# Kernel optimization log

Measured on AMD Instinct MI355X. Metric: run time of the kernel, lower is better.

## Reference

```python
import jax, jax.numpy as jnp
import numpy as np

CONF_THRES = 0.96
IOU_THRES = 0.45
MAX_CAND = 2048        # fixed candidate cap (jit-static stand-in for data-dependent nonzero)
DET_PER_IMG = 300
AGNOSTIC = False
LABEL_OFF = 4.0        # class offset for batched NMS; boxes lie within [-0.5, 1.5]


def _cxcywh_to_xyxy(b):
    cx, cy, w, h = b[..., 0], b[..., 1], b[..., 2], b[..., 3]
    return jnp.stack([cx - 0.5 * w, cy - 0.5 * h, cx + 0.5 * w, cy + 0.5 * h], axis=-1)


def _box_iou(a, b):
    # a: [K,4], b: [K,4] -> [K,K]
    lt = jnp.maximum(a[:, None, :2], b[None, :, :2])
    rb = jnp.minimum(a[:, None, 2:], b[None, :, 2:])
    wh = jnp.clip(rb - lt, 0.0)
    inter = wh[..., 0] * wh[..., 1]
    area_a = (a[:, 2] - a[:, 0]) * (a[:, 3] - a[:, 1])
    area_b = (b[:, 2] - b[:, 0]) * (b[:, 3] - b[:, 1])
    return inter / (area_a[:, None] + area_b[None, :] - inter + 1e-9)


def _process_image(x, nc):
    # x: [N, 5+nc]
    obj = x[:, 4]
    cls_scores = x[:, 5:] * obj[:, None]                 # x[:,5:] *= x[:,4:5]
    boxes = _cxcywh_to_xyxy(x[:, :4])                    # [N,4]
    # multi-label candidates: (obj > conf) pre-filter, then (obj*cls > conf)
    cand_mask = (cls_scores > CONF_THRES) & (obj[:, None] > CONF_THRES)
    flat_scores = jnp.where(cand_mask, cls_scores, -1.0).reshape(-1)  # [N*nc]
    top_scores, top_idx = jax.lax.top_k(flat_scores, MAX_CAND)        # sorted desc
    anchor = top_idx // nc
    label = top_idx % nc
    cand_boxes = boxes[anchor]                           # [K,4]
    valid = top_scores > 0.0

    # batched (class-aware) NMS via per-class coordinate offset
    if AGNOSTIC:
        nms_boxes = cand_boxes
    else:
        nms_boxes = cand_boxes + (label.astype(cand_boxes.dtype) * LABEL_OFF)[:, None]
    iou = _box_iou(nms_boxes, nms_boxes)                 # [K,K]
    idxs = jnp.arange(MAX_CAND)

    def body(i, keep):
        suppress = keep[i] & (iou[i] > IOU_THRES) & (idxs > i)
        return keep & ~suppress

    keep = jax.lax.fori_loop(0, MAX_CAND, body, valid)
    kept_scores = jnp.where(keep, top_scores, -1.0)
    det_scores, det_idx = jax.lax.top_k(kept_scores, DET_PER_IMG)
    det_valid = det_scores > 0.0
    det = jnp.concatenate(
        [cand_boxes[det_idx], det_scores[:, None], label[det_idx].astype(x.dtype)[:, None]],
        axis=1,
    )  # [DET_PER_IMG, 6] = (x1, y1, x2, y2, score, class)
    return jnp.where(det_valid[:, None], det, 0.0)


def setup_inputs() -> dict:
    key = jax.random.key(0)
    prediction = jax.random.uniform(key, (8, 25200, 85), dtype=jnp.float32)
    return {"prediction": prediction}


def reference(prediction):
    nc = prediction.shape[2] - 5
    return jax.vmap(lambda x: _process_image(x, nc))(prediction)
```

## Files before the change

kernel.cpp:

```cpp
#include <hip/hip_runtime.h>
#include <stdint.h>

#define CONF 0.96f
#define IOUT 0.45f
#define NA 25200
#define DIM 85
#define NC 80
#define NIMG 8
#define NCAND 2048
#define CAPRAW 4096
#define NDET 300
#define CH 64
#define NCH (NCAND / CH)
#define APB 112
#define NSEG (NA / APB)
#define SEGCAP 96
#define K2U 64
#define K2P 4

__global__ __launch_bounds__(128) void k1_filter(
    const float* __restrict__ pred, int* __restrict__ bcnt,
    uint64_t* __restrict__ raw_k) {
    __shared__ int   hot[APB];
    __shared__ float hobj[APB];
    __shared__ uint64_t l_k[SEGCAP];
    __shared__ int   l_hot, l_cnt;
    int tid = threadIdx.x;
    int img = blockIdx.y;
    int blk = blockIdx.x;
    int a0 = blk * APB;
    if (tid == 0) { l_hot = 0; l_cnt = 0; }
    __syncthreads();

    if (tid < APB) {
        float obj = pred[((size_t)img * NA + a0 + tid) * DIM + 4];
        if (obj > CONF) {
            int p = atomicAdd(&l_hot, 1);
            hot[p] = tid; hobj[p] = obj;
        }
    }
    __syncthreads();
    int items = l_hot * NC;
    for (int w = tid; w < items; w += 128) {
        int hi = w / NC;
        int c = w - hi * NC;
        int al = hot[hi];
        float s = pred[((size_t)img * NA + a0 + al) * DIM + 5 + c] * hobj[hi];
        if (s > CONF) {
            int q = atomicAdd(&l_cnt, 1);
            if (q < SEGCAP)
                l_k[q] = ((uint64_t)__float_as_uint(s) << 32)
                       | (uint32_t)(~(uint32_t)((a0 + al) * NC + c));
        }
    }
    __syncthreads();
    int c = l_cnt; if (c > SEGCAP) c = SEGCAP;
    if (tid == 0) bcnt[img * 256 + blk] = c;
    uint64_t* seg = raw_k + ((size_t)img * NSEG + blk) * SEGCAP;
    for (int i = tid; i < c; i += 128) seg[i] = l_k[i];
}

__global__ __launch_bounds__(256) void k2_rank(
    const float* __restrict__ pred,
    const int* __restrict__ bcnt, const uint64_t* __restrict__ raw_k,
    int* __restrict__ n_arr,
    float* __restrict__ score, int* __restrict__ label,
    float* __restrict__ ox1, float* __restrict__ oy1,
    float* __restrict__ ox2, float* __restrict__ oy2,
    float* __restrict__ area,
    float* __restrict__ rx1, float* __restrict__ ry1,
    float* __restrict__ rx2, float* __restrict__ ry2) {
    __shared__ uint64_t keys[CAPRAW];
    __shared__ int sc[256];
    __shared__ int rk[K2U][K2P];
    int img = blockIdx.y;
    int unit = blockIdx.x;
    int tid = threadIdx.x;
    int c = (tid < NSEG) ? bcnt[img * 256 + tid] : 0;
    sc[tid] = c;
    __syncthreads();
    for (int d = 1; d < 256; d <<= 1) {
        int v = (tid >= d) ? sc[tid - d] : 0;
        __syncthreads();
        sc[tid] += v;
        __syncthreads();
    }
    int total = sc[255];
    int m = total < CAPRAW ? total : CAPRAW;
    if (unit == 0 && tid == 0) n_arr[img] = m < NCAND ? m : NCAND;
    if (unit * K2U >= m) return;

    int off = sc[tid] - c;
    const uint64_t* seg = raw_k + ((size_t)img * NSEG + tid) * SEGCAP;
    for (int k = 0; k < c; ++k) {
        int pos = off + k;
        if (pos < CAPRAW) keys[pos] = seg[k];
    }
    for (int j = tid; j < CAPRAW; j += 256)
        if (j >= m) keys[j] = 0;
    __syncthreads();

    int cand = tid & (K2U - 1);
    int part = tid >> 6;
    int idx = unit * K2U + cand;
    bool valid = idx < m;
    uint64_t my = keys[idx];
    int mt = (m + 7) & ~7;
    int q = ((mt + 31) >> 5) << 3;
    int lo = part * q;
    int hi = lo + q; if (hi > mt) hi = mt;
    int r = 0;
#pragma unroll 8
    for (int j = lo; j < hi; ++j) r += (keys[j] > my) ? 1 : 0;
    rk[cand][part] = r;
    __syncthreads();
    if (part == 0) {
        int rank = rk[cand][0] + rk[cand][1] + rk[cand][2] + rk[cand][3];
        if (valid && rank < NCAND) {
            float s = __uint_as_float((uint32_t)(my >> 32));
            uint32_t myf = ~((uint32_t)my);
            int anchor = (int)(myf / NC);
            int lab = (int)(myf - (uint32_t)anchor * NC);
            const float* p = pred + ((size_t)img * NA + anchor) * DIM;
            float cx = p[0], cy = p[1], wv = p[2], hv = p[3];
            float x1 = cx - 0.5f * wv, y1 = cy - 0.5f * hv;
            float x2 = cx + 0.5f * wv, y2 = cy + 0.5f * hv;
            float offl = (float)lab * 4.0f;
            size_t o = (size_t)img * NCAND + rank;
            score[o] = s; label[o] = lab;
            rx1[o] = x1; ry1[o] = y1; rx2[o] = x2; ry2[o] = y2;
            float o1 = x1 + offl, o2 = y1 + offl, o3 = x2 + offl, o4 = y2 + offl;
            ox1[o] = o1; oy1[o] = o2; ox2[o] = o3; oy2[o] = o4;
            area[o] = (o3 - o1) * (o4 - o2);
        }
    }
}

__global__ __launch_bounds__(64) void k3_mask(
    const int* __restrict__ n_arr,
    const float* __restrict__ ox1, const float* __restrict__ oy1,
    const float* __restrict__ ox2, const float* __restrict__ oy2,
    const float* __restrict__ area, uint64_t* __restrict__ mask64) {
    __shared__ float jx1[CH], jy1[CH], jx2[CH], jy2[CH], jar[CH];
    int img = blockIdx.y;
    int n = n_arr[img];
    int ci = blockIdx.x >> 5, cj = blockIdx.x & 31;
    int t = threadIdx.x;
    size_t base = (size_t)img * NCAND;
    int i = ci * CH + t;
    uint64_t w = 0;
    if (cj >= ci && ci * CH < n && cj * CH < n) {
        {
            int j = cj * CH + t;
            float x1 = 0.f, y1 = 0.f, x2 = 0.f, y2 = 0.f, ar = 0.f;
            if (j < n) {
                x1 = ox1[base + j]; y1 = oy1[base + j];
                x2 = ox2[base + j]; y2 = oy2[base + j]; ar = area[base + j];
            }
            jx1[t] = x1; jy1[t] = y1; jx2[t] = x2; jy2[t] = y2; jar[t] = ar;
        }
        __syncthreads();
        float ax1 = 0.f, ay1 = 0.f, ax2 = 0.f, ay2 = 0.f, aar = 0.f;
        if (i < n) {
            ax1 = ox1[base + i]; ay1 = oy1[base + i];
            ax2 = ox2[base + i]; ay2 = oy2[base + i]; aar = area[base + i];
        }
        int jg0 = cj * CH;
#pragma unroll 8
        for (int jj = 0; jj < CH; ++jj) {
            float ltx = fmaxf(ax1, jx1[jj]), lty = fmaxf(ay1, jy1[jj]);
            float rbx = fminf(ax2, jx2[jj]), rby = fminf(ay2, jy2[jj]);
            float ww = fmaxf(rbx - ltx, 0.f), hh = fmaxf(rby - lty, 0.f);
            float inter = ww * hh;
            float iou = inter / (aar + jar[jj] - inter + 1e-9f);
            w |= (iou > IOUT && (jg0 + jj) > i) ? (1ull << jj) : 0ull;
        }
    }
    mask64[(base + (size_t)i) * NCH + cj] = w;
}

__global__ void k4_scan(const int* __restrict__ n_arr,
                        const uint32_t* __restrict__ mask,
                        const float* __restrict__ score, const int* __restrict__ label,
                        const float* __restrict__ rx1, const float* __restrict__ ry1,
                        const float* __restrict__ rx2, const float* __restrict__ ry2,
                        float* __restrict__ out) {
    int img = blockIdx.x;
    int lane = threadIdx.x;
    int n = n_arr[img];
    size_t cbase = (size_t)img * NCAND;
    const uint32_t* rowp = mask + cbase * 64 + lane;
    float* outp = out + (size_t)img * NDET * 6;

    uint32_t removed = 0;
    int kcnt = 0;
    constexpr int PF = 32;
    uint32_t buf[PF];
#pragma unroll
    for (int k = 0; k < PF; ++k) buf[k] = rowp[(size_t)k * 64];
    for (int ib = 0; ib < n; ib += PF) {
#pragma unroll
        for (int k = 0; k < PF; ++k) {
            int i = ib + k;
            uint32_t row = buf[k];
            int pi = i + PF; if (pi > NCAND - 1) pi = NCAND - 1;
            buf[k] = rowp[(size_t)pi * 64];
            uint32_t w = (uint32_t)__builtin_amdgcn_readlane((int)removed, i >> 5);
            uint32_t kept = ((w >> (i & 31)) & 1u) ^ 1u;
            kcnt += (int)kept;
            removed |= row & (0u - kept);
        }
        if (kcnt >= NDET) break;
    }

    int j0 = lane << 5;
    uint32_t vmask = (j0 + 32 <= n) ? 0xffffffffu
                   : (j0 >= n ? 0u : ((1u << (n - j0)) - 1u));
    uint32_t keptw = ~removed & vmask;
    int cntk = __popc(keptw);
    int pre = cntk;
    for (int d = 1; d < 64; d <<= 1) {
        int tv = __shfl_up(pre, d);
        if (lane >= d) pre += tv;
    }
    int totalk = __shfl(pre, 63);
    int r = pre - cntk;
    uint32_t wvb = keptw;
    while (wvb) {
        int b = __builtin_ctz(wvb);
        wvb &= wvb - 1;
        if (r >= NDET) break;
        int j = j0 + b;
        float* o = outp + (size_t)r * 6;
        o[0] = rx1[cbase + j]; o[1] = ry1[cbase + j];
        o[2] = rx2[cbase + j]; o[3] = ry2[cbase + j];
        o[4] = score[cbase + j]; o[5] = (float)label[cbase + j];
        ++r;
    }
    int nk = totalk < NDET ? totalk : NDET;
    for (int idx = nk * 6 + lane; idx < NDET * 6; idx += 64) outp[idx] = 0.0f;
}

extern "C" void kernel_launch(void* const* d_in, const int* in_sizes, int n_in,
                              void* d_out, int out_size, void* d_ws, size_t ws_size,
                              hipStream_t stream) {
    const float* pred = (const float*)d_in[0];
    float* out = (float*)d_out;
    char* w = (char*)d_ws;

    const size_t A_BC  = 0;
    const size_t A_RK  = 8192;
    const size_t SA    = A_RK + (size_t)NIMG * NSEG * SEGCAP * 8;
    const size_t A_N   = SA;
    const size_t SB    = SA + 256;
    const size_t SZ_S  = (size_t)NIMG * NCAND * 4;

    int*      bcnt  = (int*)(w + A_BC);
    uint64_t* raw_k = (uint64_t*)(w + A_RK);
    int*      n_arr = (int*)(w + A_N);
    float* score = (float*)(w + SB + 0 * SZ_S);
    int*   label = (int*)(w + SB + 1 * SZ_S);
    float* ox1   = (float*)(w + SB + 2 * SZ_S);
    float* oy1   = (float*)(w + SB + 3 * SZ_S);
    float* ox2   = (float*)(w + SB + 4 * SZ_S);
    float* oy2   = (float*)(w + SB + 5 * SZ_S);
    float* area  = (float*)(w + SB + 6 * SZ_S);
    float* rx1   = (float*)(w + SB + 7 * SZ_S);
    float* ry1   = (float*)(w + SB + 8 * SZ_S);
    float* rx2   = (float*)(w + SB + 9 * SZ_S);
    float* ry2   = (float*)(w + SB + 10 * SZ_S);
    uint64_t* mask64 = (uint64_t*)(w + SB + 11 * SZ_S);
    uint32_t* mask32 = (uint32_t*)mask64;

    dim3 g1(NSEG, NIMG);
    k1_filter<<<g1, 128, 0, stream>>>(pred, bcnt, raw_k);
    dim3 g2(CAPRAW / K2U, NIMG);
    k2_rank<<<g2, 256, 0, stream>>>(pred, bcnt, raw_k, n_arr,
        score, label, ox1, oy1, ox2, oy2, area, rx1, ry1, rx2, ry2);
    dim3 g3(NCH * NCH, NIMG);
    k3_mask<<<g3, CH, 0, stream>>>(n_arr, ox1, oy1, ox2, oy2, area, mask64);
    k4_scan<<<NIMG, 64, 0, stream>>>(n_arr, mask32, score, label,
        rx1, ry1, rx2, ry2, out);
}
```

Baseline: 164.3 us.

## Fuse IoU mask and NMS scan kernels via last-block atomic ticket

Merges the IoU bitmask kernel and the serial NMS scan kernel into one launch. Each 256-thread block now computes four 64x64 tiles, one per wavefront, instead of one tile per 64-thread block. An atomic per-image counter, reset in k2, picks the last-finishing block to run the greedy scan after a threadfence. This removes one kernel launch and its inter-kernel gap, at the cost of an atomic, extra fences, and the scan running on whichever CU finishes last.

```diff
diff --git a/kernel.cpp b/kernel.cpp
--- a/kernel.cpp
+++ b/kernel.cpp
@@ -17,6 +17,7 @@
 #define SEGCAP 96
 #define K2U 64
 #define K2P 4
+#define K34B 256
 
 __global__ __launch_bounds__(128) void k1_filter(
     const float* __restrict__ pred, int* __restrict__ bcnt,
@@ -63,7 +64,7 @@
 __global__ __launch_bounds__(256) void k2_rank(
     const float* __restrict__ pred,
     const int* __restrict__ bcnt, const uint64_t* __restrict__ raw_k,
-    int* __restrict__ n_arr,
+    int* __restrict__ n_arr, int* __restrict__ tick,
     float* __restrict__ score, int* __restrict__ label,
     float* __restrict__ ox1, float* __restrict__ oy1,
     float* __restrict__ ox2, float* __restrict__ oy2,
@@ -76,6 +77,7 @@
     int img = blockIdx.y;
     int unit = blockIdx.x;
     int tid = threadIdx.x;
+    if (unit == 0 && tid == 0) tick[img * 64] = 0;
     int c = (tid < NSEG) ? bcnt[img * 256 + tid] : 0;
     sc[tid] = c;
     __syncthreads();
@@ -136,30 +138,40 @@
     }
 }
 
-__global__ __launch_bounds__(64) void k3_mask(
-    const int* __restrict__ n_arr,
+__global__ __launch_bounds__(256) void k34(
+    const int* __restrict__ n_arr, int* __restrict__ tick,
     const float* __restrict__ ox1, const float* __restrict__ oy1,
     const float* __restrict__ ox2, const float* __restrict__ oy2,
-    const float* __restrict__ area, uint64_t* __restrict__ mask64) {
-    __shared__ float jx1[CH], jy1[CH], jx2[CH], jy2[CH], jar[CH];
+    const float* __restrict__ area, uint64_t* __restrict__ mask64,
+    const float* __restrict__ score, const int* __restrict__ label,
+    const float* __restrict__ rx1, const float* __restrict__ ry1,
+    const float* __restrict__ rx2, const float* __restrict__ ry2,
+    float* __restrict__ out) {
+    __shared__ float js[4][5][CH];
+    __shared__ int l_last;
     int img = blockIdx.y;
     int n = n_arr[img];
-    int ci = blockIdx.x >> 5, cj = blockIdx.x & 31;
-    int t = threadIdx.x;
+    int tid = threadIdx.x;
+    int wv = tid >> 6, lane = tid & 63;
     size_t base = (size_t)img * NCAND;
-    int i = ci * CH + t;
+
+    int T = blockIdx.x * 4 + wv;
+    int ci = T >> 5, cj = T & 31;
+    bool active = (cj >= ci) && (ci * CH < n) && (cj * CH < n);
+    if (active) {
+        int j = cj * CH + lane;
+        float x1 = 0.f, y1 = 0.f, x2 = 0.f, y2 = 0.f, ar = 0.f;
+        if (j < n) {
+            x1 = ox1[base + j]; y1 = oy1[base + j];
+            x2 = ox2[base + j]; y2 = oy2[base + j]; ar = area[base + j];
+        }
+        js[wv][0][lane] = x1; js[wv][1][lane] = y1;
+        js[wv][2][lane] = x2; js[wv][3][lane] = y2; js[wv][4][lane] = ar;
+    }
+    __syncthreads();
+    int i = ci * CH + lane;
     uint64_t w = 0;
-    if (cj >= ci && ci * CH < n && cj * CH < n) {
-        {
-            int j = cj * CH + t;
-            float x1 = 0.f, y1 = 0.f, x2 = 0.f, y2 = 0.f, ar = 0.f;
-            if (j < n) {
-                x1 = ox1[base + j]; y1 = oy1[base + j];
-                x2 = ox2[base + j]; y2 = oy2[base + j]; ar = area[base + j];
-            }
-            jx1[t] = x1; jy1[t] = y1; jx2[t] = x2; jy2[t] = y2; jar[t] = ar;
-        }
-        __syncthreads();
+    if (active) {
         float ax1 = 0.f, ay1 = 0.f, ax2 = 0.f, ay2 = 0.f, aar = 0.f;
         if (i < n) {
             ax1 = ox1[base + i]; ay1 = oy1[base + i];
@@ -168,28 +180,31 @@
         int jg0 = cj * CH;
 #pragma unroll 8
         for (int jj = 0; jj < CH; ++jj) {
-            float ltx = fmaxf(ax1, jx1[jj]), lty = fmaxf(ay1, jy1[jj]);
-            float rbx = fminf(ax2, jx2[jj]), rby = fminf(ay2, jy2[jj]);
+            float ltx = fmaxf(ax1, js[wv][0][jj]), lty = fmaxf(ay1, js[wv][1][jj]);
+            float rbx = fminf(ax2, js[wv][2][jj]), rby = fminf(ay2, js[wv][3][jj]);
             float ww = fmaxf(rbx - ltx, 0.f), hh = fmaxf(rby - lty, 0.f);
             float inter = ww * hh;
-            float iou = inter / (aar + jar[jj] - inter + 1e-9f);
+            float iou = inter / (aar + js[wv][4][jj] - inter + 1e-9f);
             w |= (iou > IOUT && (jg0 + jj) > i) ? (1ull << jj) : 0ull;
         }
     }
     mask64[(base + (size_t)i) * NCH + cj] = w;
-}
-
-__global__ void k4_scan(const int* __restrict__ n_arr,
-                        const uint32_t* __restrict__ mask,
-                        const float* __restrict__ score, const int* __restrict__ label,
-                        const float* __restrict__ rx1, const float* __restrict__ ry1,
-                        const float* __restrict__ rx2, const float* __restrict__ ry2,
-                        float* __restrict__ out) {
-    int img = blockIdx.x;
-    int lane = threadIdx.x;
-    int n = n_arr[img];
-    size_t cbase = (size_t)img * NCAND;
-    const uint32_t* rowp = mask + cbase * 64 + lane;
+
+    __threadfence();
+    __syncthreads();
+    if (tid == 0) {
+        int old = atomicAdd(&tick[img * 64], 1);
+        l_last = (old == K34B - 1) ? 1 : 0;
+    }
+    __syncthreads();
+    if (!l_last) return;
+    __threadfence();
+    if (tid >= 64) return;
+
+    const uint32_t* mask = (const uint32_t*)mask64;
+    int ln = lane;
+    size_t cbase = base;
+    const uint32_t* rowp = mask + cbase * 64 + ln;
     float* outp = out + (size_t)img * NDET * 6;
 
     uint32_t removed = 0;
@@ -201,19 +216,19 @@
     for (int ib = 0; ib < n; ib += PF) {
 #pragma unroll
         for (int k = 0; k < PF; ++k) {
-            int i = ib + k;
+            int ii = ib + k;
             uint32_t row = buf[k];
-            int pi = i + PF; if (pi > NCAND - 1) pi = NCAND - 1;
+            int pi = ii + PF; if (pi > NCAND - 1) pi = NCAND - 1;
             buf[k] = rowp[(size_t)pi * 64];
-            uint32_t w = (uint32_t)__builtin_amdgcn_readlane((int)removed, i >> 5);
-            uint32_t kept = ((w >> (i & 31)) & 1u) ^ 1u;
+            uint32_t wd = (uint32_t)__builtin_amdgcn_readlane((int)removed, ii >> 5);
+            uint32_t kept = ((wd >> (ii & 31)) & 1u) ^ 1u;
             kcnt += (int)kept;
             removed |= row & (0u - kept);
         }
         if (kcnt >= NDET) break;
     }
 
-    int j0 = lane << 5;
+    int j0 = ln << 5;
     uint32_t vmask = (j0 + 32 <= n) ? 0xffffffffu
                    : (j0 >= n ? 0u : ((1u << (n - j0)) - 1u));
     uint32_t keptw = ~removed & vmask;
@@ -221,7 +236,7 @@
     int pre = cntk;
     for (int d = 1; d < 64; d <<= 1) {
         int tv = __shfl_up(pre, d);
-        if (lane >= d) pre += tv;
+        if (ln >= d) pre += tv;
     }
     int totalk = __shfl(pre, 63);
     int r = pre - cntk;
@@ -238,7 +253,7 @@
         ++r;
     }
     int nk = totalk < NDET ? totalk : NDET;
-    for (int idx = nk * 6 + lane; idx < NDET * 6; idx += 64) outp[idx] = 0.0f;
+    for (int idx = nk * 6 + ln; idx < NDET * 6; idx += 64) outp[idx] = 0.0f;
 }
 
 extern "C" void kernel_launch(void* const* d_in, const int* in_sizes, int n_in,
@@ -252,12 +267,14 @@
     const size_t A_RK  = 8192;
     const size_t SA    = A_RK + (size_t)NIMG * NSEG * SEGCAP * 8;
     const size_t A_N   = SA;
-    const size_t SB    = SA + 256;
+    const size_t A_TK  = SA + 256;
+    const size_t SB    = A_TK + 2048;
     const size_t SZ_S  = (size_t)NIMG * NCAND * 4;
 
     int*      bcnt  = (int*)(w + A_BC);
     uint64_t* raw_k = (uint64_t*)(w + A_RK);
     int*      n_arr = (int*)(w + A_N);
+    int*      tick  = (int*)(w + A_TK);
     float* score = (float*)(w + SB + 0 * SZ_S);
     int*   label = (int*)(w + SB + 1 * SZ_S);
     float* ox1   = (float*)(w + SB + 2 * SZ_S);
@@ -270,15 +287,13 @@
     float* rx2   = (float*)(w + SB + 9 * SZ_S);
     float* ry2   = (float*)(w + SB + 10 * SZ_S);
     uint64_t* mask64 = (uint64_t*)(w + SB + 11 * SZ_S);
-    uint32_t* mask32 = (uint32_t*)mask64;
 
     dim3 g1(NSEG, NIMG);
     k1_filter<<<g1, 128, 0, stream>>>(pred, bcnt, raw_k);
     dim3 g2(CAPRAW / K2U, NIMG);
-    k2_rank<<<g2, 256, 0, stream>>>(pred, bcnt, raw_k, n_arr,
+    k2_rank<<<g2, 256, 0, stream>>>(pred, bcnt, raw_k, n_arr, tick,
         score, label, ox1, oy1, ox2, oy2, area, rx1, ry1, rx2, ry2);
-    dim3 g3(NCH * NCH, NIMG);
-    k3_mask<<<g3, CH, 0, stream>>>(n_arr, ox1, oy1, ox2, oy2, area, mask64);
-    k4_scan<<<NIMG, 64, 0, stream>>>(n_arr, mask32, score, label,
-        rx1, ry1, rx2, ry2, out);
-}
+    dim3 g3(K34B, NIMG);
+    k34<<<g3, 256, 0, stream>>>(n_arr, tick, ox1, oy1, ox2, oy2, area,
+        mask64, score, label, rx1, ry1, rx2, ry2, out);
+}
```

Measured after the change: 385.3 us. +134.5%, slower.
